# Optimization experiments

Hardware: AMD Instinct MI355X
Metric: run time of the kernel (lower is better)

The kernel has to match this reference:

```python
import jax, jax.numpy as jnp
import numpy as np
import math

NUM_HEADS = 16


def setup_inputs() -> dict:
    key = jax.random.key(0)
    ks = jax.random.split(key, 5)
    L, B, E = 2048, 2, 1024
    scale = 1.0 / math.sqrt(E)
    return {
        "query": jax.random.normal(ks[0], (L, B, E), jnp.float32),
        "key": jax.random.normal(ks[1], (L, B, E), jnp.float32),
        "value": jax.random.normal(ks[2], (L, B, E), jnp.float32),
        "in_proj_weight": jax.random.normal(ks[3], (3 * E, E), jnp.float32) * scale,
        "in_proj_bias": jnp.zeros((3 * E,), jnp.float32),
        "out_w": jax.random.normal(ks[4], (E, E), jnp.float32) * scale,
        "out_b": jnp.zeros((E,), jnp.float32),
    }


def reference(query, key, value, in_proj_weight, in_proj_bias, out_w, out_b):
    L, Bz, E = query.shape
    S = key.shape[0]
    H = NUM_HEADS
    hd = E // H
    # in-projection: chunk packed weight into q/k/v parts (same math as torch chunk)
    w_q, w_k, w_v = jnp.split(in_proj_weight, 3, axis=0)
    b_q, b_k, b_v = jnp.split(in_proj_bias, 3, axis=0)
    q = query @ w_q.T + b_q            # (L, B, E)
    k = key @ w_k.T + b_k              # (S, B, E)
    v = value @ w_v.T + b_v            # (S, B, E)
    # (L, B*H, hd) -> (B*H, L, hd)
    q = q.reshape(L, Bz * H, hd).transpose(1, 0, 2) / math.sqrt(hd)
    k = k.reshape(S, Bz * H, hd).transpose(1, 0, 2)
    v = v.reshape(S, Bz * H, hd).transpose(1, 0, 2)
    # sigmoid attention (non-softmax), full (B*H, L, S) matrix as in original
    attn = jax.nn.sigmoid(jnp.einsum("bld,bsd->bls", q, k))
    denom = attn.sum(axis=-1, keepdims=True) + 1e-4
    out = jnp.einsum("bls,bsd->bld", attn / denom, v)  # (B*H, L, hd)
    out = out.transpose(1, 0, 2).reshape(L, Bz, E)
    out = out @ out_w.T + out_b
    avg_weights = attn.reshape(Bz, H, L, S).sum(axis=1) / H
    return out, avg_weights
```

## Files before the change

kernel.cpp:

```cpp
#include <hip/hip_runtime.h>
#include <stdint.h>


#define L_SEQ 2048
#define NBATCH 2
#define EMB 1024
#define NHEAD 16
#define HD 64
#define MROWS 4096

typedef __bf16 bf16x8 __attribute__((ext_vector_type(8)));
typedef float f32x4 __attribute__((ext_vector_type(4)));
typedef float f32x16 __attribute__((ext_vector_type(16)));

__device__ __forceinline__ unsigned short f2bf(float f) {
  union { float f; uint32_t u; } v; v.f = f;
  uint32_t u = v.u;
  u += 0x7fffu + ((u >> 16) & 1u);
  return (unsigned short)(u >> 16);
}

__device__ __forceinline__ unsigned short f2bf_fast(float f) {
  union { float f; uint32_t u; } v; v.f = f;
  return (unsigned short)((v.u + 0x8000u) >> 16);
}

__device__ __forceinline__ void gl_lds16(const void* gptr, void* ldsptr) {
  const uint32_t* g = reinterpret_cast<const uint32_t*>(gptr);
  auto* l = reinterpret_cast<__attribute__((address_space(3))) uint32_t*>(
      reinterpret_cast<uintptr_t>(ldsptr));
  __builtin_amdgcn_global_load_lds(g, l, 16, 0, 0);
}

__device__ __forceinline__ f32x4 mfma16(bf16x8 a, bf16x8 b, f32x4 c) {
  return __builtin_amdgcn_mfma_f32_16x16x32_bf16(a, b, c, 0, 0, 0);
}

__device__ __forceinline__ f32x16 mfma32(bf16x8 a, bf16x8 b, f32x16 c) {
  return __builtin_amdgcn_mfma_f32_32x32x16_bf16(a, b, c, 0, 0, 0);
}

__device__ __forceinline__ float fast_sigmoid(float x) {
  float e = __expf(-x);
  return __builtin_amdgcn_rcpf(1.0f + e);
}

__global__ __launch_bounds__(256) void k_convert(
    const float* __restrict__ qin, const float* __restrict__ kin,
    const float* __restrict__ vin, const float* __restrict__ win,
    const float* __restrict__ wo,
    unsigned short* __restrict__ Xq, unsigned short* __restrict__ Xk,
    unsigned short* __restrict__ Xv, unsigned short* __restrict__ Wb,
    unsigned short* __restrict__ Wob) {
  const int row = blockIdx.x;
  const int t = threadIdx.x;
  const float* src;
  unsigned short* dst;
  int srow;
  size_t drow;
  if (row < 3 * MROWS) {
    const int which = row >> 12;
    const int m = row & (MROWS - 1);
    const int b = m >> 11, l = m & (L_SEQ - 1);
    srow = l * NBATCH + b;
    drow = (size_t)m;
    src = which == 0 ? qin : (which == 1 ? kin : vin);
    dst = which == 0 ? Xq : (which == 1 ? Xk : Xv);
  } else if (row < 3 * MROWS + 3072) {
    srow = row - 3 * MROWS; drow = (size_t)srow; src = win; dst = Wb;
  } else {
    srow = row - (3 * MROWS + 3072); drow = (size_t)srow; src = wo; dst = Wob;
  }
  const float4 vv = *(const float4*)(src + (size_t)srow * EMB + t * 4);
  ushort4 o;
  o.x = f2bf(vv.x); o.y = f2bf(vv.y); o.z = f2bf(vv.z); o.w = f2bf(vv.w);
  *(ushort4*)(dst + drow * EMB + t * 4) = o;
}

__device__ __forceinline__ void gemm_core(
    const unsigned short* __restrict__ A, const unsigned short* __restrict__ Bm,
    int m0, int n0, unsigned short* sA, unsigned short* sB, f32x4 acc[4][4]) {
  const int tid = threadIdx.x;
  const int wave = tid >> 6;
  const int lane = tid & 63;
  const int quad = lane >> 4;
  const int l16 = lane & 15;
  const int wm = (wave >> 1) * 64;
  const int wn = (wave & 1) * 64;
  const int srow = lane >> 2;
  const int scol = lane & 3;

  for (int mi = 0; mi < 4; ++mi)
    for (int ni = 0; ni < 4; ++ni)
      acc[mi][ni] = (f32x4){0.f, 0.f, 0.f, 0.f};

  for (int k0 = 0; k0 < EMB; k0 += 32) {
    __syncthreads();
    for (int i = 0; i < 2; ++i) {
      const int p = wave * 2 + i;
      const int r = p * 16 + srow;
      const int c = scol ^ ((r >> 1) & 3);
      gl_lds16(A + (size_t)(m0 + r) * EMB + k0 + c * 8, sA + p * 512);
      gl_lds16(Bm + (size_t)(n0 + r) * EMB + k0 + c * 8, sB + p * 512);
    }
    __syncthreads();
    bf16x8 af[4], bfr[4];
    for (int mi = 0; mi < 4; ++mi) {
      const int r = wm + mi * 16 + l16;
      const int cp = quad ^ ((r >> 1) & 3);
      af[mi] = *(const bf16x8*)(sA + r * 32 + cp * 8);
    }
    for (int ni = 0; ni < 4; ++ni) {
      const int r = wn + ni * 16 + l16;
      const int cp = quad ^ ((r >> 1) & 3);
      bfr[ni] = *(const bf16x8*)(sB + r * 32 + cp * 8);
    }
    for (int mi = 0; mi < 4; ++mi)
      for (int ni = 0; ni < 4; ++ni)
        acc[mi][ni] = mfma16(af[mi], bfr[ni], acc[mi][ni]);
  }
}

__global__ __launch_bounds__(256) void k_inproj(
    const unsigned short* __restrict__ Xq, const unsigned short* __restrict__ Xk,
    const unsigned short* __restrict__ Xv, const unsigned short* __restrict__ Wb,
    const float* __restrict__ bias,
    unsigned short* __restrict__ qb, unsigned short* __restrict__ kb,
    unsigned short* __restrict__ vb) {
  __shared__ __attribute__((aligned(16))) unsigned short sA[128 * 32];
  __shared__ __attribute__((aligned(16))) unsigned short sB[128 * 32];
  __shared__ __attribute__((aligned(16))) unsigned short sT[128 * 128];
  const int z = blockIdx.z;
  const unsigned short* A = z == 0 ? Xq : (z == 1 ? Xk : Xv);
  const int n0 = blockIdx.x * 128, m0 = blockIdx.y * 128;
  f32x4 acc[4][4];
  gemm_core(A, Wb + (size_t)z * EMB * EMB, m0, n0, sA, sB, acc);

  const int tid = threadIdx.x, wave = tid >> 6, lane = tid & 63;
  const int quad = lane >> 4, l16 = lane & 15;
  const int wm = (wave >> 1) * 64, wn = (wave & 1) * 64;
  const int bb = m0 >> 11, lbase = m0 & (L_SEQ - 1);

  if (z == 2) {
    for (int ni = 0; ni < 4; ++ni) {
      const int n = wn + ni * 16 + l16;
      const float bv = bias[2 * EMB + n0 + n];
      const int x = (n & 15) << 1;
      for (int mi = 0; mi < 4; ++mi) {
        const int mchunk = ((wm + mi * 16) >> 2) + quad;
        const int slot = mchunk ^ x;
        ushort4 pk;
        pk.x = f2bf(acc[mi][ni][0] + bv);
        pk.y = f2bf(acc[mi][ni][1] + bv);
        pk.z = f2bf(acc[mi][ni][2] + bv);
        pk.w = f2bf(acc[mi][ni][3] + bv);
        *(ushort4*)(sT + (size_t)n * 128 + slot * 4) = pk;
      }
    }
    __syncthreads();
    const int n = tid >> 1, hf = tid & 1;
    const int ng = n0 + n;
    const int h = ng >> 6, d = ng & 63;
    unsigned short* dst =
        vb + ((size_t)(bb * NHEAD + h) * HD + d) * L_SEQ + lbase + hf * 64;
    const int x = (n & 15) << 1;
    for (int j = 0; j < 8; ++j) {
      const int c2 = hf * 16 + j * 2;
      const int slot = c2 ^ x;
      uint4 vd = *(const uint4*)(sT + (size_t)n * 128 + slot * 4);
      *(uint4*)(dst + j * 8) = vd;
    }
  } else {
    const float scale = (z == 0) ? 0.125f : 1.0f;
    unsigned short* dst01 = (z == 0) ? qb : kb;
    for (int ni = 0; ni < 4; ++ni) {
      const int n = n0 + wn + ni * 16 + l16;
      const float bv = bias[z * EMB + n];
      const int h = n >> 6, d = n & 63;
      for (int mi = 0; mi < 4; ++mi) {
        for (int r = 0; r < 4; ++r) {
          const int m = m0 + wm + mi * 16 + quad * 4 + r;
          const int b = m >> 11, l = m & (L_SEQ - 1);
          dst01[((size_t)(b * NHEAD + h) * L_SEQ + l) * HD + d] =
              f2bf((acc[mi][ni][r] + bv) * scale);
        }
      }
    }
  }
}

__global__ __launch_bounds__(512) void k_attn(
    const unsigned short* __restrict__ qb, const unsigned short* __restrict__ kb,
    const unsigned short* __restrict__ vb, unsigned short* __restrict__ oh) {
  __shared__ __attribute__((aligned(16))) unsigned short sQ[128 * 64];
  __shared__ __attribute__((aligned(16))) unsigned short sK[2][64 * 64];
  __shared__ __attribute__((aligned(16))) unsigned short sV[2][64 * 64];
  __shared__ __attribute__((aligned(16))) unsigned short sP[128 * 72];

  const int bh = blockIdx.x;
  const int b = bh >> 4, h = bh & 15;
  const int l0 = blockIdx.y * 128;
  const unsigned short* qg = qb + ((size_t)bh * L_SEQ + l0) * HD;
  const unsigned short* kg = kb + (size_t)bh * L_SEQ * HD;
  const unsigned short* vg = vb + (size_t)bh * HD * L_SEQ;

  const int tid = threadIdx.x, wave = tid >> 6, lane = tid & 63;
  const int quad = lane >> 4, l16 = lane & 15;
  const int l32 = lane & 31, lh = lane >> 5;
  const int sr8 = lane >> 3, sc8 = lane & 7;
  const int sh = (wave >> 2) * 32;
  const int lq = (wave & 3) * 32;
  const int lt = wave & 3;
  const int dt = wave >> 2;

  for (int i = 0; i < 2; ++i) {
    const int p = wave * 2 + i;
    const int r = p * 8 + sr8;
    const int c = sc8 ^ (r & 7);
    gl_lds16(qg + (size_t)r * HD + c * 8, sQ + p * 512);
  }
  if (wave < 4) {
    for (int i = 0; i < 2; ++i) {
      const int p = wave * 2 + i;
      const int r = p * 8 + sr8;
      const int c = sc8 ^ (r & 7);
      gl_lds16(kg + (size_t)r * HD + c * 8, sK[0] + p * 512);
    }
  } else {
    for (int i = 0; i < 2; ++i) {
      const int p = (wave - 4) * 2 + i;
      const int r = p * 8 + sr8;
      const int c = sc8 ^ (r & 7);
      gl_lds16(vg + (size_t)r * L_SEQ + c * 8, sV[0] + p * 512);
    }
  }

  f32x16 oacc, dacc;
  for (int i = 0; i < 16; ++i) { oacc[i] = 0.f; dacc[i] = 0.f; }
  bf16x8 ones;
  for (int j = 0; j < 8; ++j) ones[j] = (__bf16)1.0f;

  for (int it = 0; it < 32; ++it) {
    __syncthreads();
    const int cur = it & 1;
    if (it < 31) {
      const int nxt = cur ^ 1;
      const int s1 = (it + 1) * 64;
      if (wave < 4) {
        for (int i = 0; i < 2; ++i) {
          const int p = wave * 2 + i;
          const int r = p * 8 + sr8;
          const int c = sc8 ^ (r & 7);
          gl_lds16(kg + (size_t)(s1 + r) * HD + c * 8, sK[nxt] + p * 512);
        }
      } else {
        for (int i = 0; i < 2; ++i) {
          const int p = (wave - 4) * 2 + i;
          const int r = p * 8 + sr8;
          const int c = sc8 ^ (r & 7);
          gl_lds16(vg + (size_t)r * L_SEQ + s1 + c * 8, sV[nxt] + p * 512);
        }
      }
    }

    f32x4 st[2][2];
    for (int smi = 0; smi < 2; ++smi)
      for (int lni = 0; lni < 2; ++lni) st[smi][lni] = (f32x4){0.f, 0.f, 0.f, 0.f};
    for (int kk = 0; kk < HD; kk += 32) {
      bf16x8 a[2], bq[2];
      for (int smi = 0; smi < 2; ++smi) {
        const int r = sh + smi * 16 + l16;
        const int c = ((kk >> 3) + quad) ^ (r & 7);
        a[smi] = *(const bf16x8*)(sK[cur] + r * 64 + c * 8);
      }
      for (int lni = 0; lni < 2; ++lni) {
        const int r = lq + lni * 16 + l16;
        const int c = ((kk >> 3) + quad) ^ (r & 7);
        bq[lni] = *(const bf16x8*)(sQ + r * 64 + c * 8);
      }
      for (int smi = 0; smi < 2; ++smi)
        for (int lni = 0; lni < 2; ++lni)
          st[smi][lni] = mfma16(a[smi], bq[lni], st[smi][lni]);
    }

    for (int lni = 0; lni < 2; ++lni) {
      const int lrow = lq + lni * 16 + l16;
      for (int smi = 0; smi < 2; ++smi) {
        uint32_t u[4];
        for (int r = 0; r < 4; ++r) {
          union { float f; uint32_t i; } cv;
          cv.f = fast_sigmoid(st[smi][lni][r]);
          u[r] = cv.i + 0x8000u;
        }
        uint2 pk;
        pk.x = __builtin_amdgcn_perm(u[1], u[0], 0x07060302u);
        pk.y = __builtin_amdgcn_perm(u[3], u[2], 0x07060302u);
        *(uint2*)(sP + (size_t)lrow * 72 + sh + smi * 16 + quad * 4) = pk;
      }
    }
    __syncthreads();

    const unsigned short* prow = sP + (size_t)(lt * 32 + l32) * 72;
    const int vrow = dt * 32 + l32;
    for (int kk = 0; kk < 4; ++kk) {
      bf16x8 ap = *(const bf16x8*)(prow + kk * 16 + lh * 8);
      const int c = (kk * 2 + lh) ^ (vrow & 7);
      bf16x8 bv = *(const bf16x8*)(sV[cur] + vrow * 64 + c * 8);
      oacc = mfma32(ap, bv, oacc);
      dacc = mfma32(ap, ones, dacc);
    }
  }

  for (int r = 0; r < 16; ++r) {
    const int row = (r & 3) + 8 * (r >> 2) + 4 * lh;
    const int l = l0 + lt * 32 + row;
    const float rden = __builtin_amdgcn_rcpf(dacc[r] + 1e-4f);
    oh[((size_t)(b * L_SEQ + l)) * EMB + h * HD + dt * 32 + l32] =
        f2bf_fast(oacc[r] * rden);
  }
}

__global__ __launch_bounds__(512) void k_avg(
    const unsigned short* __restrict__ qb, const unsigned short* __restrict__ kb,
    float* __restrict__ avg) {
  __shared__ __attribute__((aligned(16))) unsigned short sQ[2][128 * 64];
  __shared__ __attribute__((aligned(16))) unsigned short sK[2][256 * 64];
  const int ss0 = blockIdx.x * 256, l0 = blockIdx.y * 128, b = blockIdx.z;
  const int tid = threadIdx.x, wave = tid >> 6, lane = tid & 63;
  const int l32 = lane & 31, lh = lane >> 5;
  const int sr8 = lane >> 3, sc8 = lane & 7;
  const int mt = wave & 3;
  const int ntg = (wave >> 2) * 4;

  const unsigned short* qg0 = qb + ((size_t)(b * NHEAD) * L_SEQ + l0) * HD;
  const unsigned short* kg0 = kb + ((size_t)(b * NHEAD) * L_SEQ + ss0) * HD;
  const size_t hstride = (size_t)L_SEQ * HD;

  for (int i = 0; i < 2; ++i) {
    const int p = wave * 2 + i;
    const int r = p * 8 + sr8;
    const int c = sc8 ^ (r & 7);
    gl_lds16(qg0 + (size_t)r * HD + c * 8, sQ[0] + p * 512);
  }
  for (int i = 0; i < 4; ++i) {
    const int p = wave * 4 + i;
    const int r = p * 8 + sr8;
    const int c = sc8 ^ (r & 7);
    gl_lds16(kg0 + (size_t)r * HD + c * 8, sK[0] + p * 512);
  }

  f32x16 av[4];
  for (int t = 0; t < 4; ++t)
    for (int i = 0; i < 16; ++i) av[t][i] = 0.f;

  for (int h = 0; h < NHEAD; ++h) {
    __syncthreads();
    const int cur = h & 1;
    if (h < NHEAD - 1) {
      const int nxt = cur ^ 1;
      const unsigned short* qg = qg0 + (size_t)(h + 1) * hstride;
      const unsigned short* kg = kg0 + (size_t)(h + 1) * hstride;
      for (int i = 0; i < 2; ++i) {
        const int p = wave * 2 + i;
        const int r = p * 8 + sr8;
        const int c = sc8 ^ (r & 7);
        gl_lds16(qg + (size_t)r * HD + c * 8, sQ[nxt] + p * 512);
      }
      for (int i = 0; i < 4; ++i) {
        const int p = wave * 4 + i;
        const int r = p * 8 + sr8;
        const int c = sc8 ^ (r & 7);
        gl_lds16(kg + (size_t)r * HD + c * 8, sK[nxt] + p * 512);
      }
    }

    f32x16 scr[4];
    for (int t = 0; t < 4; ++t)
      for (int i = 0; i < 16; ++i) scr[t][i] = 0.f;
    const int qrow = mt * 32 + l32;
    for (int kk = 0; kk < 4; ++kk) {
      const int cq = (kk * 2 + lh) ^ (qrow & 7);
      bf16x8 aq = *(const bf16x8*)(sQ[cur] + qrow * 64 + cq * 8);
      for (int t = 0; t < 4; ++t) {
        const int krow = (ntg + t) * 32 + l32;
        const int ck = (kk * 2 + lh) ^ (krow & 7);
        bf16x8 bk = *(const bf16x8*)(sK[cur] + krow * 64 + ck * 8);
        scr[t] = mfma32(aq, bk, scr[t]);
      }
    }
    for (int t = 0; t < 4; ++t)
      for (int r = 0; r < 16; ++r)
        av[t][r] += fast_sigmoid(scr[t][r]);
  }

  for (int t = 0; t < 4; ++t) {
    for (int r = 0; r < 16; ++r) {
      const int l = l0 + mt * 32 + (r & 3) + 8 * (r >> 2) + 4 * lh;
      const int s = ss0 + (ntg + t) * 32 + l32;
      avg[((size_t)b * L_SEQ + l) * L_SEQ + s] = av[t][r] * 0.0625f;
    }
  }
}

__global__ __launch_bounds__(256) void k_outproj(
    const unsigned short* __restrict__ OH, const unsigned short* __restrict__ Wob,
    const float* __restrict__ ob, float* __restrict__ out) {
  __shared__ __attribute__((aligned(16))) unsigned short sA[128 * 32];
  __shared__ __attribute__((aligned(16))) unsigned short sB[128 * 32];
  const int n0 = blockIdx.x * 128, m0 = blockIdx.y * 128;
  f32x4 acc[4][4];
  gemm_core(OH, Wob, m0, n0, sA, sB, acc);

  const int tid = threadIdx.x, wave = tid >> 6, lane = tid & 63;
  const int quad = lane >> 4, l16 = lane & 15;
  const int wm = (wave >> 1) * 64, wn = (wave & 1) * 64;
  for (int ni = 0; ni < 4; ++ni) {
    const int n = n0 + wn + ni * 16 + l16;
    const float bv = ob[n];
    for (int mi = 0; mi < 4; ++mi) {
      for (int r = 0; r < 4; ++r) {
        const int m = m0 + wm + mi * 16 + quad * 4 + r;
        const int b = m >> 11, l = m & (L_SEQ - 1);
        out[((size_t)l * NBATCH + b) * EMB + n] = acc[mi][ni][r] + bv;
      }
    }
  }
}

extern "C" void kernel_launch(void* const* d_in, const int* in_sizes, int n_in,
                              void* d_out, int out_size, void* d_ws, size_t ws_size,
                              hipStream_t stream) {
  (void)in_sizes; (void)n_in; (void)out_size;
  const float* qin = (const float*)d_in[0];
  const float* kin = (const float*)d_in[1];
  const float* vin = (const float*)d_in[2];
  const float* w   = (const float*)d_in[3];
  const float* bias = (const float*)d_in[4];
  const float* wo  = (const float*)d_in[5];
  const float* ob  = (const float*)d_in[6];
  float* out = (float*)d_out;

  unsigned short* Xq  = (unsigned short*)d_ws;
  unsigned short* Xk  = Xq + (size_t)MROWS * EMB;
  unsigned short* Xv  = Xk + (size_t)MROWS * EMB;
  unsigned short* Wb  = Xv + (size_t)MROWS * EMB;
  unsigned short* Wob = Wb + (size_t)3 * EMB * EMB;
  unsigned short* qbuf = Wob + (size_t)EMB * EMB;
  unsigned short* kbuf = qbuf + (size_t)MROWS * EMB;
  unsigned short* vbuf = kbuf + (size_t)MROWS * EMB;
  unsigned short* ohb  = vbuf + (size_t)MROWS * EMB;
  const size_t need = ((size_t)MROWS * EMB * 7 + (size_t)4 * EMB * EMB) * 2;
  if (ws_size < need) return;

  k_convert<<<16384, 256, 0, stream>>>(qin, kin, vin, w, wo, Xq, Xk, Xv, Wb, Wob);
  k_inproj<<<dim3(8, 32, 3), 256, 0, stream>>>(Xq, Xk, Xv, Wb, bias, qbuf, kbuf, vbuf);
  k_attn<<<dim3(32, 16), 512, 0, stream>>>(qbuf, kbuf, vbuf, ohb);
  k_avg<<<dim3(8, 16, 2), 512, 0, stream>>>(qbuf, kbuf, out + (size_t)MROWS * EMB);
  k_outproj<<<dim3(8, 32), 256, 0, stream>>>(ohb, Wob, ob, out);
}
```

Baseline: 290.1 us.

## Stage Q/K projection stores via LDS, restructure attention PV tiling, shrink avg tiles

The in-projection epilogue for Q and K now writes into a swizzled LDS tile and then emits coalesced 16-byte global stores, and the V transpose store is reorganised so that each thread issues one 16-byte store per row pass. The attention kernel drops K/V double buffering in favour of a single buffer with two barriers per step, and switches the P·V product from 32x32 to 16x16 MFMA tiles with per-wave row ownership. The averaged-weights kernel halves its S tile per block and doubles the grid to raise occupancy. Removing the prefetch exposes global-load latency in the attention loop, which may offset the gains elsewhere.

```diff
diff --git a/kernel.cpp b/kernel.cpp
--- a/kernel.cpp
+++ b/kernel.cpp
@@ -140,6 +140,7 @@
   const int quad = lane >> 4, l16 = lane & 15;
   const int wm = (wave >> 1) * 64, wn = (wave & 1) * 64;
   const int bb = m0 >> 11, lbase = m0 & (L_SEQ - 1);
+  const int lane8 = tid & 7, rowid = tid >> 3;
 
   if (z == 2) {
     for (int ni = 0; ni < 4; ++ni) {
@@ -158,33 +159,47 @@
       }
     }
     __syncthreads();
-    const int n = tid >> 1, hf = tid & 1;
-    const int ng = n0 + n;
-    const int h = ng >> 6, d = ng & 63;
-    unsigned short* dst =
-        vb + ((size_t)(bb * NHEAD + h) * HD + d) * L_SEQ + lbase + hf * 64;
-    const int x = (n & 15) << 1;
-    for (int j = 0; j < 8; ++j) {
-      const int c2 = hf * 16 + j * 2;
+    for (int p = 0; p < 8; ++p) {
+      const int row = rowid + p * 32;
+      const int n = row >> 1, hf = row & 1;
+      const int x = (n & 15) << 1;
+      const int c2 = hf * 16 + lane8 * 2;
       const int slot = c2 ^ x;
       uint4 vd = *(const uint4*)(sT + (size_t)n * 128 + slot * 4);
-      *(uint4*)(dst + j * 8) = vd;
+      const int ng = n0 + n;
+      const int h = ng >> 6, d = ng & 63;
+      unsigned short* dst =
+          vb + ((size_t)(bb * NHEAD + h) * HD + d) * L_SEQ + lbase + hf * 64;
+      *(uint4*)(dst + lane8 * 8) = vd;
     }
   } else {
     const float scale = (z == 0) ? 0.125f : 1.0f;
-    unsigned short* dst01 = (z == 0) ? qb : kb;
+    unsigned short* dstp = (z == 0) ? qb : kb;
     for (int ni = 0; ni < 4; ++ni) {
-      const int n = n0 + wn + ni * 16 + l16;
-      const float bv = bias[z * EMB + n];
-      const int h = n >> 6, d = n & 63;
+      const int n = wn + ni * 16 + l16;
+      const float bv = bias[z * EMB + n0 + n];
       for (int mi = 0; mi < 4; ++mi) {
         for (int r = 0; r < 4; ++r) {
-          const int m = m0 + wm + mi * 16 + quad * 4 + r;
-          const int b = m >> 11, l = m & (L_SEQ - 1);
-          dst01[((size_t)(b * NHEAD + h) * L_SEQ + l) * HD + d] =
+          const int m = wm + mi * 16 + quad * 4 + r;
+          const int g = (m >> 2) & 7;
+          sT[(size_t)m * 128 + (n ^ (g << 4))] =
               f2bf((acc[mi][ni][r] + bv) * scale);
         }
       }
+    }
+    __syncthreads();
+    for (int p = 0; p < 8; ++p) {
+      const int row = rowid + p * 32;
+      const int l = row >> 1, hf = row & 1;
+      const int g2 = ((l >> 2) & 7) << 1;
+      const int c = hf * 8 + lane8;
+      const int slot = c ^ g2;
+      uint4 vd = *(const uint4*)(sT + (size_t)l * 128 + slot * 8);
+      const int ng = n0 + c * 8;
+      const int h = ng >> 6, d = ng & 63;
+      unsigned short* dst =
+          dstp + ((size_t)(bb * NHEAD + h) * L_SEQ + lbase + l) * HD + d;
+      *(uint4*)dst = vd;
     }
   }
 }
@@ -193,8 +208,8 @@
     const unsigned short* __restrict__ qb, const unsigned short* __restrict__ kb,
     const unsigned short* __restrict__ vb, unsigned short* __restrict__ oh) {
   __shared__ __attribute__((aligned(16))) unsigned short sQ[128 * 64];
-  __shared__ __attribute__((aligned(16))) unsigned short sK[2][64 * 64];
-  __shared__ __attribute__((aligned(16))) unsigned short sV[2][64 * 64];
+  __shared__ __attribute__((aligned(16))) unsigned short sK[64 * 64];
+  __shared__ __attribute__((aligned(16))) unsigned short sV[64 * 64];
   __shared__ __attribute__((aligned(16))) unsigned short sP[128 * 72];
 
   const int bh = blockIdx.x;
@@ -206,12 +221,9 @@
 
   const int tid = threadIdx.x, wave = tid >> 6, lane = tid & 63;
   const int quad = lane >> 4, l16 = lane & 15;
-  const int l32 = lane & 31, lh = lane >> 5;
   const int sr8 = lane >> 3, sc8 = lane & 7;
   const int sh = (wave >> 2) * 32;
   const int lq = (wave & 3) * 32;
-  const int lt = wave & 3;
-  const int dt = wave >> 2;
 
   for (int i = 0; i < 2; ++i) {
     const int p = wave * 2 + i;
@@ -219,49 +231,32 @@
     const int c = sc8 ^ (r & 7);
     gl_lds16(qg + (size_t)r * HD + c * 8, sQ + p * 512);
   }
-  if (wave < 4) {
-    for (int i = 0; i < 2; ++i) {
-      const int p = wave * 2 + i;
-      const int r = p * 8 + sr8;
-      const int c = sc8 ^ (r & 7);
-      gl_lds16(kg + (size_t)r * HD + c * 8, sK[0] + p * 512);
-    }
-  } else {
-    for (int i = 0; i < 2; ++i) {
-      const int p = (wave - 4) * 2 + i;
-      const int r = p * 8 + sr8;
-      const int c = sc8 ^ (r & 7);
-      gl_lds16(vg + (size_t)r * L_SEQ + c * 8, sV[0] + p * 512);
-    }
-  }
-
-  f32x16 oacc, dacc;
-  for (int i = 0; i < 16; ++i) { oacc[i] = 0.f; dacc[i] = 0.f; }
+
+  f32x4 oacc[4];
+  for (int ni = 0; ni < 4; ++ni) oacc[ni] = (f32x4){0.f, 0.f, 0.f, 0.f};
+  f32x4 dacc = (f32x4){0.f, 0.f, 0.f, 0.f};
+
   bf16x8 ones;
   for (int j = 0; j < 8; ++j) ones[j] = (__bf16)1.0f;
 
-  for (int it = 0; it < 32; ++it) {
-    __syncthreads();
-    const int cur = it & 1;
-    if (it < 31) {
-      const int nxt = cur ^ 1;
-      const int s1 = (it + 1) * 64;
-      if (wave < 4) {
-        for (int i = 0; i < 2; ++i) {
-          const int p = wave * 2 + i;
-          const int r = p * 8 + sr8;
-          const int c = sc8 ^ (r & 7);
-          gl_lds16(kg + (size_t)(s1 + r) * HD + c * 8, sK[nxt] + p * 512);
-        }
-      } else {
-        for (int i = 0; i < 2; ++i) {
-          const int p = (wave - 4) * 2 + i;
-          const int r = p * 8 + sr8;
-          const int c = sc8 ^ (r & 7);
-          gl_lds16(vg + (size_t)r * L_SEQ + s1 + c * 8, sV[nxt] + p * 512);
-        }
-      }
-    }
+  for (int s0 = 0; s0 < L_SEQ; s0 += 64) {
+    __syncthreads();
+    if (wave < 4) {
+      for (int i = 0; i < 2; ++i) {
+        const int p = wave * 2 + i;
+        const int r = p * 8 + sr8;
+        const int c = sc8 ^ (r & 7);
+        gl_lds16(kg + (size_t)(s0 + r) * HD + c * 8, sK + p * 512);
+      }
+    } else {
+      for (int i = 0; i < 2; ++i) {
+        const int p = (wave - 4) * 2 + i;
+        const int r = p * 8 + sr8;
+        const int c = sc8 ^ (r & 7);
+        gl_lds16(vg + (size_t)r * L_SEQ + s0 + c * 8, sV + p * 512);
+      }
+    }
+    __syncthreads();
 
     f32x4 st[2][2];
     for (int smi = 0; smi < 2; ++smi)
@@ -271,7 +266,7 @@
       for (int smi = 0; smi < 2; ++smi) {
         const int r = sh + smi * 16 + l16;
         const int c = ((kk >> 3) + quad) ^ (r & 7);
-        a[smi] = *(const bf16x8*)(sK[cur] + r * 64 + c * 8);
+        a[smi] = *(const bf16x8*)(sK + r * 64 + c * 8);
       }
       for (int lni = 0; lni < 2; ++lni) {
         const int r = lq + lni * 16 + l16;
@@ -300,23 +295,25 @@
     }
     __syncthreads();
 
-    const unsigned short* prow = sP + (size_t)(lt * 32 + l32) * 72;
-    const int vrow = dt * 32 + l32;
-    for (int kk = 0; kk < 4; ++kk) {
-      bf16x8 ap = *(const bf16x8*)(prow + kk * 16 + lh * 8);
-      const int c = (kk * 2 + lh) ^ (vrow & 7);
-      bf16x8 bv = *(const bf16x8*)(sV[cur] + vrow * 64 + c * 8);
-      oacc = mfma32(ap, bv, oacc);
-      dacc = mfma32(ap, ones, dacc);
-    }
-  }
-
-  for (int r = 0; r < 16; ++r) {
-    const int row = (r & 3) + 8 * (r >> 2) + 4 * lh;
-    const int l = l0 + lt * 32 + row;
+    const int lr = wave * 16 + l16;
+    for (int kk = 0; kk < 64; kk += 32) {
+      bf16x8 ap = *(const bf16x8*)(sP + (size_t)lr * 72 + kk + quad * 8);
+      for (int ni = 0; ni < 4; ++ni) {
+        const int rd = ni * 16 + l16;
+        const int c = ((kk >> 3) + quad) ^ (rd & 7);
+        bf16x8 bv4 = *(const bf16x8*)(sV + rd * 64 + c * 8);
+        oacc[ni] = mfma16(ap, bv4, oacc[ni]);
+      }
+      dacc = mfma16(ap, ones, dacc);
+    }
+  }
+
+  for (int r = 0; r < 4; ++r) {
+    const int lrow = l0 + wave * 16 + quad * 4 + r;
     const float rden = __builtin_amdgcn_rcpf(dacc[r] + 1e-4f);
-    oh[((size_t)(b * L_SEQ + l)) * EMB + h * HD + dt * 32 + l32] =
-        f2bf_fast(oacc[r] * rden);
+    unsigned short* dst = oh + ((size_t)(b * L_SEQ + lrow)) * EMB + h * HD;
+    for (int ni = 0; ni < 4; ++ni)
+      dst[ni * 16 + l16] = f2bf_fast(oacc[ni][r] * rden);
   }
 }
 
@@ -324,13 +321,13 @@
     const unsigned short* __restrict__ qb, const unsigned short* __restrict__ kb,
     float* __restrict__ avg) {
   __shared__ __attribute__((aligned(16))) unsigned short sQ[2][128 * 64];
-  __shared__ __attribute__((aligned(16))) unsigned short sK[2][256 * 64];
-  const int ss0 = blockIdx.x * 256, l0 = blockIdx.y * 128, b = blockIdx.z;
+  __shared__ __attribute__((aligned(16))) unsigned short sK[2][128 * 64];
+  const int ss0 = blockIdx.x * 128, l0 = blockIdx.y * 128, b = blockIdx.z;
   const int tid = threadIdx.x, wave = tid >> 6, lane = tid & 63;
   const int l32 = lane & 31, lh = lane >> 5;
   const int sr8 = lane >> 3, sc8 = lane & 7;
   const int mt = wave & 3;
-  const int ntg = (wave >> 2) * 4;
+  const int ntg = (wave >> 2) * 2;
 
   const unsigned short* qg0 = qb + ((size_t)(b * NHEAD) * L_SEQ + l0) * HD;
   const unsigned short* kg0 = kb + ((size_t)(b * NHEAD) * L_SEQ + ss0) * HD;
@@ -341,16 +338,11 @@
     const int r = p * 8 + sr8;
     const int c = sc8 ^ (r & 7);
     gl_lds16(qg0 + (size_t)r * HD + c * 8, sQ[0] + p * 512);
-  }
-  for (int i = 0; i < 4; ++i) {
-    const int p = wave * 4 + i;
-    const int r = p * 8 + sr8;
-    const int c = sc8 ^ (r & 7);
     gl_lds16(kg0 + (size_t)r * HD + c * 8, sK[0] + p * 512);
   }
 
-  f32x16 av[4];
-  for (int t = 0; t < 4; ++t)
+  f32x16 av[2];
+  for (int t = 0; t < 2; ++t)
     for (int i = 0; i < 16; ++i) av[t][i] = 0.f;
 
   for (int h = 0; h < NHEAD; ++h) {
@@ -365,35 +357,30 @@
         const int r = p * 8 + sr8;
         const int c = sc8 ^ (r & 7);
         gl_lds16(qg + (size_t)r * HD + c * 8, sQ[nxt] + p * 512);
-      }
-      for (int i = 0; i < 4; ++i) {
-        const int p = wave * 4 + i;
-        const int r = p * 8 + sr8;
-        const int c = sc8 ^ (r & 7);
         gl_lds16(kg + (size_t)r * HD + c * 8, sK[nxt] + p * 512);
       }
     }
 
-    f32x16 scr[4];
-    for (int t = 0; t < 4; ++t)
+    f32x16 scr[2];
+    for (int t = 0; t < 2; ++t)
       for (int i = 0; i < 16; ++i) scr[t][i] = 0.f;
     const int qrow = mt * 32 + l32;
     for (int kk = 0; kk < 4; ++kk) {
       const int cq = (kk * 2 + lh) ^ (qrow & 7);
       bf16x8 aq = *(const bf16x8*)(sQ[cur] + qrow * 64 + cq * 8);
-      for (int t = 0; t < 4; ++t) {
+      for (int t = 0; t < 2; ++t) {
         const int krow = (ntg + t) * 32 + l32;
         const int ck = (kk * 2 + lh) ^ (krow & 7);
         bf16x8 bk = *(const bf16x8*)(sK[cur] + krow * 64 + ck * 8);
         scr[t] = mfma32(aq, bk, scr[t]);
       }
     }
-    for (int t = 0; t < 4; ++t)
+    for (int t = 0; t < 2; ++t)
       for (int r = 0; r < 16; ++r)
         av[t][r] += fast_sigmoid(scr[t][r]);
   }
 
-  for (int t = 0; t < 4; ++t) {
+  for (int t = 0; t < 2; ++t) {
     for (int r = 0; r < 16; ++r) {
       const int l = l0 + mt * 32 + (r & 3) + 8 * (r >> 2) + 4 * lh;
       const int s = ss0 + (ntg + t) * 32 + l32;
@@ -455,6 +442,6 @@
   k_convert<<<16384, 256, 0, stream>>>(qin, kin, vin, w, wo, Xq, Xk, Xv, Wb, Wob);
   k_inproj<<<dim3(8, 32, 3), 256, 0, stream>>>(Xq, Xk, Xv, Wb, bias, qbuf, kbuf, vbuf);
   k_attn<<<dim3(32, 16), 512, 0, stream>>>(qbuf, kbuf, vbuf, ohb);
-  k_avg<<<dim3(8, 16, 2), 512, 0, stream>>>(qbuf, kbuf, out + (size_t)MROWS * EMB);
+  k_avg<<<dim3(16, 16, 2), 512, 0, stream>>>(qbuf, kbuf, out + (size_t)MROWS * EMB);
   k_outproj<<<dim3(8, 32), 256, 0, stream>>>(ohb, Wob, ob, out);
 }
```

Result: faster. 284.0 us (-2.1%).
